# Kernel tuning notes

Measured on AMD Instinct MI355X. Metric: run time of the kernel, lower is better.

## Reference

```python
import jax, jax.numpy as jnp
import numpy as np

N_NODES = 100000
N_EDGES = 1600000
IN_F = 128
HID = 16
NEG_SLOPE = 0.2


def setup_inputs() -> dict:
    key = jax.random.key(0)
    ks = jax.random.split(key, 12)
    x = jax.random.normal(ks[0], (N_NODES, IN_F), dtype=jnp.float32)
    edge_index = jax.random.randint(ks[1], (2, N_EDGES), 0, N_NODES, dtype=jnp.int32)
    s1 = 1.0 / np.sqrt(IN_F)
    s2 = 1.0 / np.sqrt(2 * HID)
    # layer 1: heads=2, out=16, concat -> 32
    W1 = jax.random.normal(ks[2], (IN_F, 2 * HID), dtype=jnp.float32) * s1
    a_src1 = jax.random.normal(ks[3], (2, HID), dtype=jnp.float32) * s2
    a_dst1 = jax.random.normal(ks[4], (2, HID), dtype=jnp.float32) * s2
    b1 = jnp.zeros((2 * HID,), dtype=jnp.float32)
    # layer 2: heads=1, out=1
    W2 = jax.random.normal(ks[5], (2 * HID, 1), dtype=jnp.float32) * s2
    a_src2 = jax.random.normal(ks[6], (1, 1), dtype=jnp.float32)
    a_dst2 = jax.random.normal(ks[7], (1, 1), dtype=jnp.float32)
    b2 = jnp.zeros((1,), dtype=jnp.float32)
    return {"x": x, "edge_index": edge_index, "W1": W1, "a_src1": a_src1,
            "a_dst1": a_dst1, "b1": b1, "W2": W2, "a_src2": a_src2,
            "a_dst2": a_dst2, "b2": b2}


def gat_conv(x, src, dst, W, a_src, a_dst, bias, heads, out_ch, concat):
    # PyG GATConv: linear proj, per-edge leaky-relu score, segment softmax over
    # incoming edges (dst), scatter-add aggregation. Self loops already in src/dst.
    n = x.shape[0]
    h = (x @ W).reshape(n, heads, out_ch)                      # [N,H,C]
    alpha_s = (h * a_src[None]).sum(-1)                        # [N,H]
    alpha_d = (h * a_dst[None]).sum(-1)                        # [N,H]
    e = jax.nn.leaky_relu(alpha_s[src] + alpha_d[dst], NEG_SLOPE)  # [E,H]
    m = jax.lax.stop_gradient(jax.ops.segment_max(e, dst, num_segments=n))
    ex = jnp.exp(e - m[dst])
    denom = jax.ops.segment_sum(ex, dst, num_segments=n)       # [N,H]
    alpha = ex / (denom[dst] + 1e-16)                          # [E,H]
    out = jax.ops.segment_sum(alpha[..., None] * h[src], dst, num_segments=n)  # [N,H,C]
    out = out.reshape(n, heads * out_ch) if concat else out.mean(axis=1)
    return out + bias


def reference(x, edge_index, W1, a_src1, a_dst1, b1, W2, a_src2, a_dst2, b2):
    n = x.shape[0]
    loop = jnp.arange(n, dtype=edge_index.dtype)
    src = jnp.concatenate([edge_index[0], loop])
    dst = jnp.concatenate([edge_index[1], loop])
    h = jax.nn.elu(gat_conv(x, src, dst, W1, a_src1, a_dst1, b1, 2, HID, True))
    out = gat_conv(h, src, dst, W2, a_src2, a_dst2, b2, 1, 1, False)
    return out
```

## Files before the change

kernel.cpp:

```cpp
#include <hip/hip_runtime.h>
#include <math.h>

#define IN_F 128
#define C1 32
#define NEG 0.2f
#define BSZ 128
#define CAP 2560
#define EPB 2048
#define TPW 2

typedef _Float16 h16;
typedef _Float16 h16x2 __attribute__((ext_vector_type(2)));
typedef _Float16 h16x4 __attribute__((ext_vector_type(4)));
typedef _Float16 h16x8 __attribute__((ext_vector_type(8)));
typedef float f32x4 __attribute__((ext_vector_type(4)));

__device__ __forceinline__ float leaky(float x) { return x >= 0.f ? x : NEG * x; }

__global__ __launch_bounds__(256)
void k_fat(const float* __restrict__ x, const float* __restrict__ W1,
           const float* __restrict__ a_s, const float* __restrict__ a_d,
           h16* __restrict__ h1h, float* __restrict__ as1,
           float* __restrict__ ad1, int N,
           const int* __restrict__ ei, int E, int ET, int nbk,
           int* __restrict__ bcnt, int* __restrict__ ebuf, int nproj) {
    __shared__ int smem[6144];
    int t = threadIdx.x;
    if ((int)blockIdx.x < nproj) {
        int wid = t >> 6, lane = t & 63;
        int q = lane >> 4, r = lane & 15;
        h16x8 Bf[2][4];
        #pragma unroll
        for (int ct = 0; ct < 2; ++ct)
            #pragma unroll
            for (int kc = 0; kc < 4; ++kc)
                #pragma unroll
                for (int j = 0; j < 8; ++j)
                    Bf[ct][kc][j] = (h16)W1[(kc * 32 + q * 8 + j) * C1 + ct * 16 + r];
        float a_s0 = a_s[r], a_s1v = a_s[16 + r];
        float a_d0 = a_d[r], a_d1v = a_d[16 + r];
        #pragma unroll
        for (int tt = 0; tt < TPW; ++tt) {
            int tile = (blockIdx.x * 4 + wid) * TPW + tt;
            int m0 = tile << 4;
            if (m0 >= N) break;
            int row = m0 + r; if (row >= N) row = N - 1;
            const float* xr = x + (size_t)row * IN_F + q * 8;
            f32x4 acc0 = {0.f, 0.f, 0.f, 0.f};
            f32x4 acc1 = {0.f, 0.f, 0.f, 0.f};
            #pragma unroll
            for (int kc = 0; kc < 4; ++kc) {
                float4 xa = *(const float4*)(xr + kc * 32);
                float4 xb = *(const float4*)(xr + kc * 32 + 4);
                h16x8 A;
                A[0] = (h16)xa.x; A[1] = (h16)xa.y; A[2] = (h16)xa.z; A[3] = (h16)xa.w;
                A[4] = (h16)xb.x; A[5] = (h16)xb.y; A[6] = (h16)xb.z; A[7] = (h16)xb.w;
                acc0 = __builtin_amdgcn_mfma_f32_16x16x32_f16(A, Bf[0][kc], acc0, 0, 0, 0);
                acc1 = __builtin_amdgcn_mfma_f32_16x16x32_f16(A, Bf[1][kc], acc1, 0, 0, 0);
            }
            #pragma unroll
            for (int reg = 0; reg < 4; ++reg) {
                int node = m0 + q * 4 + reg;
                bool vld = node < N;
                float h0 = acc0[reg], h1 = acc1[reg];
                if (vld) {
                    h1h[(size_t)node * C1 + r]      = (h16)h0;
                    h1h[(size_t)node * C1 + 16 + r] = (h16)h1;
                }
                float s0 = h0 * a_s0, s1 = h1 * a_s1v;
                float d0 = h0 * a_d0, d1 = h1 * a_d1v;
                s0 += __shfl_xor(s0, 1); s0 += __shfl_xor(s0, 2); s0 += __shfl_xor(s0, 4); s0 += __shfl_xor(s0, 8);
                s1 += __shfl_xor(s1, 1); s1 += __shfl_xor(s1, 2); s1 += __shfl_xor(s1, 4); s1 += __shfl_xor(s1, 8);
                d0 += __shfl_xor(d0, 1); d0 += __shfl_xor(d0, 2); d0 += __shfl_xor(d0, 4); d0 += __shfl_xor(d0, 8);
                d1 += __shfl_xor(d1, 1); d1 += __shfl_xor(d1, 2); d1 += __shfl_xor(d1, 4); d1 += __shfl_xor(d1, 8);
                if (vld && r == 0) {
                    *(float2*)&as1[node * 2] = make_float2(s0, s1);
                    *(float2*)&ad1[node * 2] = make_float2(d0, d1);
                }
            }
        }
    } else {
        int* hist = smem;
        int* lcur = hist + 1024;
        int2* ecache = (int2*)(lcur + 1024);
        int bid = blockIdx.x - nproj;
        hist[t] = 0; hist[t + 256] = 0; hist[t + 512] = 0; hist[t + 768] = 0;
        __syncthreads();
        int i0 = bid * EPB, i1 = min(ET, i0 + EPB);
        for (int i = i0 + t; i < i1; i += 256) {
            int s, d;
            if (i < E) { s = ei[i]; d = ei[E + i]; } else { s = d = i - E; }
            ecache[i - i0] = make_int2(s, d);
            atomicAdd(&hist[d >> 7], 1);
        }
        __syncthreads();
        for (int b = t; b < nbk; b += 256) {
            int h = hist[b];
            int base = h ? atomicAdd(&bcnt[b], h) : 0;
            lcur[b] = b * CAP + base;
        }
        __syncthreads();
        for (int i = i0 + t; i < i1; i += 256) {
            int2 e = ecache[i - i0];
            int bkt = e.y >> 7;
            int pos = atomicAdd(&lcur[bkt], 1);
            if (pos < (bkt + 1) * CAP)
                ebuf[pos] = (e.x << 7) | (e.y & 127);
        }
    }
}

__global__ __launch_bounds__(512)
void k_bagg(const int* __restrict__ bcnt, const int* __restrict__ ebuf,
            int N, int nbk, int ET,
            const float* __restrict__ as1, const float* __restrict__ ad1,
            const float* __restrict__ b1, const float* __restrict__ W2,
            const h16* __restrict__ h1h, int* __restrict__ off,
            int* __restrict__ csr1, float* __restrict__ p2) {
    __shared__ int2 elist[CAP];
    __shared__ int deg[BSZ], sst[BSZ], cur[BSZ];
    __shared__ float adl[BSZ * 2];
    __shared__ int red[8];
    int b = blockIdx.x, t = threadIdx.x;
    int cnt = min(bcnt[b], CAP);
    int ebase = b * CAP;
    int n0 = b * BSZ;
    int part = 0;
    for (int k = t; k < b; k += 512) part += min(bcnt[k], CAP);
    part += __shfl_xor(part, 1);  part += __shfl_xor(part, 2);
    part += __shfl_xor(part, 4);  part += __shfl_xor(part, 8);
    part += __shfl_xor(part, 16); part += __shfl_xor(part, 32);
    if ((t & 63) == 0) red[t >> 6] = part;
    if (t < BSZ) {
        deg[t] = 0;
        int n = n0 + t;
        float2 v = (n < N) ? ((const float2*)ad1)[n] : make_float2(0.f, 0.f);
        adl[t * 2] = v.x; adl[t * 2 + 1] = v.y;
    }
    __syncthreads();
    int fbase = red[0] + red[1] + red[2] + red[3] + red[4] + red[5] + red[6] + red[7];
    if (b == nbk - 1 && t == 0) off[N] = ET;
    for (int i = t; i < cnt; i += 512)
        atomicAdd(&deg[ebuf[ebase + i] & 127], 1);
    __syncthreads();
    int v = (t < BSZ) ? deg[t] : 0;
    __syncthreads();
    for (int o = 1; o < BSZ; o <<= 1) {
        int xv = (t >= o && t < BSZ) ? deg[t - o] : 0;
        __syncthreads();
        if (t < BSZ) deg[t] += xv;
        __syncthreads();
    }
    if (t < BSZ) {
        int excl = deg[t] - v;
        sst[t] = excl; cur[t] = excl;
        if (n0 + t < N) off[n0 + t] = fbase + excl;
    }
    __syncthreads();
    for (int i = t; i < cnt; i += 512) {
        int e = ebuf[ebase + i];
        int dl = e & 127, s = e >> 7;
        float2 asv = ((const float2*)as1)[s];
        float w0 = __expf(leaky(asv.x + adl[dl * 2 + 0]));
        float w1 = __expf(leaky(asv.y + adl[dl * 2 + 1]));
        h16x2 wp = { (h16)w0, (h16)w1 };
        int p = atomicAdd(&cur[dl], 1);
        int2 rec; rec.x = s; rec.y = *(int*)&wp;
        elist[p] = rec;
        csr1[fbase + p] = s;
    }
    __syncthreads();
    int l = t & 7, slot = t >> 3, c0 = l * 4, head = l >> 2;
    float b1l[4] = { b1[c0], b1[c0 + 1], b1[c0 + 2], b1[c0 + 3] };
    float w2l[4] = { W2[c0], W2[c0 + 1], W2[c0 + 2], W2[c0 + 3] };
    #pragma unroll
    for (int pass = 0; pass < 2; ++pass) {
        int dl = pass * 64 + slot;
        int node = n0 + dl;
        if (node >= N) break;
        int j0 = sst[dl], j1 = deg[dl];
        float den = 0.f, a0 = 0.f, a1 = 0.f, a2 = 0.f, a3 = 0.f;
        for (int j = j0; j < j1; j += 4) {
            #pragma unroll
            for (int k = 0; k < 4; ++k) {
                int jj = j + k;
                bool valid = jj < j1;
                jj = valid ? jj : j0;
                int2 e = elist[jj];
                int s = e.x;
                h16x2 wv = *(h16x2*)&e.y;
                float w = valid ? (float)(head ? wv.y : wv.x) : 0.f;
                h16x4 hv = *(const h16x4*)(h1h + ((size_t)s << 5) + c0);
                den += w;
                a0 = fmaf(w, (float)hv.x, a0);
                a1 = fmaf(w, (float)hv.y, a1);
                a2 = fmaf(w, (float)hv.z, a2);
                a3 = fmaf(w, (float)hv.w, a3);
            }
        }
        float inv = 1.f / (den + 1e-16f);
        float o, val = 0.f;
        o = a0 * inv + b1l[0]; o = o > 0.f ? o : expm1f(o); val = fmaf(o, w2l[0], val);
        o = a1 * inv + b1l[1]; o = o > 0.f ? o : expm1f(o); val = fmaf(o, w2l[1], val);
        o = a2 * inv + b1l[2]; o = o > 0.f ? o : expm1f(o); val = fmaf(o, w2l[2], val);
        o = a3 * inv + b1l[3]; o = o > 0.f ? o : expm1f(o); val = fmaf(o, w2l[3], val);
        val += __shfl_xor(val, 1); val += __shfl_xor(val, 2); val += __shfl_xor(val, 4);
        if (l == 0) p2[node] = val;
    }
}

__global__ void k_l2(const int* __restrict__ off, const int* __restrict__ csr1,
                     const float* __restrict__ p2, const float* __restrict__ as2,
                     const float* __restrict__ ad2, const float* __restrict__ b2,
                     float* __restrict__ out, int N) {
    int i = blockIdx.x * blockDim.x + threadIdx.x;
    if (i >= N) return;
    float A = as2[0];
    float Bc = ad2[0] * p2[i];
    float den = 0.f, num = 0.f;
    int j0 = off[i], j1 = off[i + 1];
    for (int j = j0; j < j1; j += 4) {
        #pragma unroll
        for (int k = 0; k < 4; ++k) {
            int jj = j + k;
            bool valid = jj < j1;
            int s = csr1[valid ? jj : j0];
            float ps = p2[s];
            float w = valid ? __expf(leaky(fmaf(ps, A, Bc))) : 0.f;
            den += w;
            num = fmaf(w, ps, num);
        }
    }
    out[i] = num / (den + 1e-16f) + b2[0];
}

extern "C" void kernel_launch(void* const* d_in, const int* in_sizes, int n_in,
                              void* d_out, int out_size, void* d_ws, size_t ws_size,
                              hipStream_t stream) {
    const float* x    = (const float*)d_in[0];
    const int*   ei   = (const int*)d_in[1];
    const float* W1   = (const float*)d_in[2];
    const float* a_s1 = (const float*)d_in[3];
    const float* a_d1 = (const float*)d_in[4];
    const float* b1   = (const float*)d_in[5];
    const float* W2   = (const float*)d_in[6];
    const float* a_s2 = (const float*)d_in[7];
    const float* a_d2 = (const float*)d_in[8];
    const float* b2   = (const float*)d_in[9];
    float* out = (float*)d_out;

    const int N  = in_sizes[0] / IN_F;
    const int E  = in_sizes[1] / 2;
    const int ET = E + N;
    const int nbk = (N + BSZ - 1) / BSZ;

    float* w   = (float*)d_ws;
    float* as1 = w; w += (size_t)2 * N;
    float* ad1 = w; w += (size_t)2 * N;
    float* p2  = w; w += (size_t)N;
    h16* h1h   = (h16*)w;
    w += (size_t)16 * N;
    int* iw     = (int*)w;
    int* bcnt   = iw; iw += 1024;
    int* off    = iw; iw += (N + 1);
    int* csr1   = iw; iw += ET;
    int* ebuf   = iw; iw += (size_t)nbk * CAP;

    const int B = 256;
    const int ntile = (N + 15) / 16;
    const int nproj = (ntile + 4 * TPW - 1) / (4 * TPW);
    const int nblkA = (ET + EPB - 1) / EPB;

    hipMemsetAsync(bcnt, 0, 1024 * sizeof(int), stream);
    k_fat <<<nproj + nblkA, B, 0, stream>>>(x, W1, a_s1, a_d1, h1h, as1, ad1, N,
                                            ei, E, ET, nbk, bcnt, ebuf, nproj);
    k_bagg<<<nbk, 512, 0, stream>>>(bcnt, ebuf, N, nbk, ET, as1, ad1, b1, W2,
                                    h1h, off, csr1, p2);
    k_l2  <<<(N + B - 1) / B, B, 0, stream>>>(off, csr1, p2, a_s2, a_d2, b2, out, N);
}
```

Baseline: 180.9 us.

## Drop LDS edge cache, widen layer-1 gather lanes, split layer-2 node across 4 lanes

The edge-bucketing path stops caching edges in shared memory and rereads edge_index from global in the scatter pass, cutting LDS use from 24KB to 8KB so more blocks can be resident. The layer-1 aggregation now gives each node 4 lanes that each load 8 halfs, instead of 8 lanes with 4 halfs over two passes, so every thread handles one node. Layer-2 aggregation gives each node 4 lanes with a shuffle reduction instead of one thread per node. This aims to raise occupancy and memory-level parallelism, at the cost of an extra global read of the edge indices.

```diff
diff --git a/kernel.cpp b/kernel.cpp
--- a/kernel.cpp
+++ b/kernel.cpp
@@ -24,7 +24,7 @@
            float* __restrict__ ad1, int N,
            const int* __restrict__ ei, int E, int ET, int nbk,
            int* __restrict__ bcnt, int* __restrict__ ebuf, int nproj) {
-    __shared__ int smem[6144];
+    __shared__ int smem[2048];
     int t = threadIdx.x;
     if ((int)blockIdx.x < nproj) {
         int wid = t >> 6, lane = t & 63;
@@ -82,15 +82,12 @@
     } else {
         int* hist = smem;
         int* lcur = hist + 1024;
-        int2* ecache = (int2*)(lcur + 1024);
         int bid = blockIdx.x - nproj;
         hist[t] = 0; hist[t + 256] = 0; hist[t + 512] = 0; hist[t + 768] = 0;
         __syncthreads();
         int i0 = bid * EPB, i1 = min(ET, i0 + EPB);
         for (int i = i0 + t; i < i1; i += 256) {
-            int s, d;
-            if (i < E) { s = ei[i]; d = ei[E + i]; } else { s = d = i - E; }
-            ecache[i - i0] = make_int2(s, d);
+            int d = (i < E) ? ei[E + i] : i - E;
             atomicAdd(&hist[d >> 7], 1);
         }
         __syncthreads();
@@ -101,11 +98,12 @@
         }
         __syncthreads();
         for (int i = i0 + t; i < i1; i += 256) {
-            int2 e = ecache[i - i0];
-            int bkt = e.y >> 7;
+            int s, d;
+            if (i < E) { s = ei[i]; d = ei[E + i]; } else { s = d = i - E; }
+            int bkt = d >> 7;
             int pos = atomicAdd(&lcur[bkt], 1);
             if (pos < (bkt + 1) * CAP)
-                ebuf[pos] = (e.x << 7) | (e.y & 127);
+                ebuf[pos] = (s << 7) | (d & 127);
         }
     }
 }
@@ -170,68 +168,69 @@
         csr1[fbase + p] = s;
     }
     __syncthreads();
-    int l = t & 7, slot = t >> 3, c0 = l * 4, head = l >> 2;
-    float b1l[4] = { b1[c0], b1[c0 + 1], b1[c0 + 2], b1[c0 + 3] };
-    float w2l[4] = { W2[c0], W2[c0 + 1], W2[c0 + 2], W2[c0 + 3] };
+    int l = t & 3, dl = t >> 2, c0 = l * 8, head = l >> 1;
+    int node = n0 + dl;
+    if (node >= N) return;
+    int j0 = sst[dl], j1 = deg[dl];
+    float den = 0.f;
+    float acc[8];
     #pragma unroll
-    for (int pass = 0; pass < 2; ++pass) {
-        int dl = pass * 64 + slot;
-        int node = n0 + dl;
-        if (node >= N) break;
-        int j0 = sst[dl], j1 = deg[dl];
-        float den = 0.f, a0 = 0.f, a1 = 0.f, a2 = 0.f, a3 = 0.f;
-        for (int j = j0; j < j1; j += 4) {
-            #pragma unroll
-            for (int k = 0; k < 4; ++k) {
-                int jj = j + k;
-                bool valid = jj < j1;
-                jj = valid ? jj : j0;
-                int2 e = elist[jj];
-                int s = e.x;
-                h16x2 wv = *(h16x2*)&e.y;
-                float w = valid ? (float)(head ? wv.y : wv.x) : 0.f;
-                h16x4 hv = *(const h16x4*)(h1h + ((size_t)s << 5) + c0);
-                den += w;
-                a0 = fmaf(w, (float)hv.x, a0);
-                a1 = fmaf(w, (float)hv.y, a1);
-                a2 = fmaf(w, (float)hv.z, a2);
-                a3 = fmaf(w, (float)hv.w, a3);
-            }
-        }
-        float inv = 1.f / (den + 1e-16f);
-        float o, val = 0.f;
-        o = a0 * inv + b1l[0]; o = o > 0.f ? o : expm1f(o); val = fmaf(o, w2l[0], val);
-        o = a1 * inv + b1l[1]; o = o > 0.f ? o : expm1f(o); val = fmaf(o, w2l[1], val);
-        o = a2 * inv + b1l[2]; o = o > 0.f ? o : expm1f(o); val = fmaf(o, w2l[2], val);
-        o = a3 * inv + b1l[3]; o = o > 0.f ? o : expm1f(o); val = fmaf(o, w2l[3], val);
-        val += __shfl_xor(val, 1); val += __shfl_xor(val, 2); val += __shfl_xor(val, 4);
-        if (l == 0) p2[node] = val;
-    }
-}
-
-__global__ void k_l2(const int* __restrict__ off, const int* __restrict__ csr1,
-                     const float* __restrict__ p2, const float* __restrict__ as2,
-                     const float* __restrict__ ad2, const float* __restrict__ b2,
-                     float* __restrict__ out, int N) {
-    int i = blockIdx.x * blockDim.x + threadIdx.x;
-    if (i >= N) return;
-    float A = as2[0];
-    float Bc = ad2[0] * p2[i];
-    float den = 0.f, num = 0.f;
-    int j0 = off[i], j1 = off[i + 1];
+    for (int c = 0; c < 8; ++c) acc[c] = 0.f;
     for (int j = j0; j < j1; j += 4) {
         #pragma unroll
         for (int k = 0; k < 4; ++k) {
             int jj = j + k;
             bool valid = jj < j1;
-            int s = csr1[valid ? jj : j0];
-            float ps = p2[s];
-            float w = valid ? __expf(leaky(fmaf(ps, A, Bc))) : 0.f;
+            jj = valid ? jj : j0;
+            int2 e = elist[jj];
+            int s = e.x;
+            h16x2 wv = *(h16x2*)&e.y;
+            float w = valid ? (float)(head ? wv.y : wv.x) : 0.f;
+            h16x8 hv = *(const h16x8*)(h1h + ((size_t)s << 5) + c0);
             den += w;
-            num = fmaf(w, ps, num);
-        }
-    }
-    out[i] = num / (den + 1e-16f) + b2[0];
+            #pragma unroll
+            for (int c = 0; c < 8; ++c) acc[c] = fmaf(w, (float)hv[c], acc[c]);
+        }
+    }
+    float inv = 1.f / (den + 1e-16f);
+    float val = 0.f;
+    #pragma unroll
+    for (int c = 0; c < 8; ++c) {
+        float o = acc[c] * inv + b1[c0 + c];
+        o = o > 0.f ? o : expm1f(o);
+        val = fmaf(o, W2[c0 + c], val);
+    }
+    val += __shfl_xor(val, 1); val += __shfl_xor(val, 2);
+    if (l == 0) p2[node] = val;
+}
+
+__global__ __launch_bounds__(256)
+void k_l2(const int* __restrict__ off, const int* __restrict__ csr1,
+          const float* __restrict__ p2, const float* __restrict__ as2,
+          const float* __restrict__ ad2, const float* __restrict__ b2,
+          float* __restrict__ out, int N) {
+    int t = threadIdx.x;
+    int node = blockIdx.x * 64 + (t >> 2);
+    if (node >= N) return;
+    int l = t & 3;
+    float A = as2[0];
+    float Bc = ad2[0] * p2[node];
+    float den = 0.f, num = 0.f;
+    int j0 = off[node], j1 = off[node + 1];
+    for (int j = j0 + l; j < j1; j += 8) {
+        int s0 = csr1[j];
+        int jb = j + 4;
+        bool vb = jb < j1;
+        int s1 = csr1[vb ? jb : j];
+        float ps0 = p2[s0], ps1 = p2[s1];
+        float w0 = __expf(leaky(fmaf(ps0, A, Bc)));
+        float w1 = vb ? __expf(leaky(fmaf(ps1, A, Bc))) : 0.f;
+        den += w0 + w1;
+        num = fmaf(w0, ps0, fmaf(w1, ps1, num));
+    }
+    den += __shfl_xor(den, 1); den += __shfl_xor(den, 2);
+    num += __shfl_xor(num, 1); num += __shfl_xor(num, 2);
+    if (l == 0) out[node] = num / (den + 1e-16f) + b2[0];
 }
 
 extern "C" void kernel_launch(void* const* d_in, const int* in_sizes, int n_in,
@@ -276,5 +275,5 @@
                                             ei, E, ET, nbk, bcnt, ebuf, nproj);
     k_bagg<<<nbk, 512, 0, stream>>>(bcnt, ebuf, N, nbk, ET, as1, ad1, b1, W2,
                                     h1h, off, csr1, p2);
-    k_l2  <<<(N + B - 1) / B, B, 0, stream>>>(off, csr1, p2, a_s2, a_d2, b2, out, N);
-}
+    k_l2  <<<(N + 63) / 64, B, 0, stream>>>(off, csr1, p2, a_s2, a_d2, b2, out, N);
+}
```

Measured after the change: 184.0 us. No clear change (+1.7%).
